# Optimization experiments

Hardware: AMD Instinct MI355X
Metric: run time of the kernel (lower is better)

Reference implementation:

```python
import jax, jax.numpy as jnp
import numpy as np

WINDOW = (16, 16)
STRIDE = (8, 8)
PADDING = (0, 0)  # (pad_h, pad_w), applied symmetrically like torch _pair semantics


def setup_inputs() -> dict:
    key = jax.random.key(0)
    x = jax.random.normal(key, (16, 3, 512, 512), dtype=jnp.float32)
    return {"x": x}


def reference(x) -> jnp.ndarray:
    wh, ww = WINDOW
    sh, sw = STRIDE
    ph, pw = PADDING
    if ph or pw:
        x = jnp.pad(x, ((0, 0), (0, 0), (ph, ph), (pw, pw)))
    B, C, H, W = x.shape
    nH = (H - wh) // sh + 1
    nW = (W - ww) // sw + 1
    # overlapping window gather indices
    rows = (jnp.arange(nH) * sh)[:, None] + jnp.arange(wh)[None, :]  # (nH, wh)
    cols = (jnp.arange(nW) * sw)[:, None] + jnp.arange(ww)[None, :]  # (nW, ww)
    # gather: (B, C, nH, nW, wh, ww)
    p = x[:, :, rows[:, None, :, None], cols[None, :, None, :]]
    # permute to (B, nH, nW, C, wh, ww) then flatten patch grid -> (B, N, C, wh, ww)
    p = jnp.transpose(p, (0, 2, 3, 1, 4, 5))
    return p.reshape(B, nH * nW, C, wh, ww)
```

## Files before the change

kernel.cpp:

```cpp
#include <hip/hip_runtime.h>


#define BB 16
#define CC 3
#define HH 512
#define WW 512
#define NH 63
#define NW 63
#define NP (NH * NW)
#define WIN 16
#define STR 8
#define LDSW 520

typedef float f4 __attribute__((ext_vector_type(4)));

__global__ __launch_bounds__(256) void extract_patches_lds(
    const float* __restrict__ x, float* __restrict__ out) {
  __shared__ float lds[WIN * LDSW];

  unsigned int blk = blockIdx.x;
  unsigned int ph = blk % NH;
  unsigned int t2 = blk / NH;
  unsigned int c  = t2 % CC;
  unsigned int b  = t2 / CC;
  unsigned int tid = threadIdx.x;

  const f4* src = reinterpret_cast<const f4*>(
      x + (((size_t)(b * CC + c) * HH + ph * STR) * WW));
  #pragma unroll
  for (int k = 0; k < 8; ++k) {
    unsigned int idx  = tid + k * 256u;
    f4 v = src[idx];
    unsigned int row  = idx >> 7;
    unsigned int col4 = idx & 127u;
    *reinterpret_cast<f4*>(&lds[row * LDSW + col4 * 4u]) = v;
  }
  __syncthreads();

  f4* dst = reinterpret_cast<f4*>(out) +
            (((size_t)b * NP + (size_t)ph * NW) * CC + c) * 64u;
  for (unsigned int u = tid; u < NW * 64u; u += 256u) {
    unsigned int pw = u >> 6;
    unsigned int r  = u & 63u;
    unsigned int i  = r >> 2;
    unsigned int j4 = r & 3u;
    f4 v = *reinterpret_cast<const f4*>(&lds[i * LDSW + pw * STR + j4 * 4u]);
    __builtin_nontemporal_store(v, &dst[(size_t)pw * (CC * 64u) + r]);
  }
}

extern "C" void kernel_launch(void* const* d_in, const int* in_sizes, int n_in,
                              void* d_out, int out_size, void* d_ws, size_t ws_size,
                              hipStream_t stream) {
  const float* x = (const float*)d_in[0];
  float* out = (float*)d_out;
  dim3 grid(BB * CC * NH);
  extract_patches_lds<<<grid, 256, 0, stream>>>(x, out);
}
```

Baseline: 227.1 us.

## Replace LDS gather with per-element scatter of input to all patch copies

Each thread now loads one float4 of the input exactly once and writes it directly to up to four output positions, the overlapping patches that contain it. The LDS staging, barrier and re-reading of overlapping rows are gone, so total input reads drop to a single pass. In exchange, output writes become scattered 16-byte stores across distant patch addresses instead of contiguous per-row patch runs, which may hurt write coalescing.

```diff
diff --git a/kernel.cpp b/kernel.cpp
--- a/kernel.cpp
+++ b/kernel.cpp
@@ -8,45 +8,43 @@
 #define NH 63
 #define NW 63
 #define NP (NH * NW)
-#define WIN 16
-#define STR 8
-#define LDSW 520
 
 typedef float f4 __attribute__((ext_vector_type(4)));
 
-__global__ __launch_bounds__(256) void extract_patches_lds(
+__global__ __launch_bounds__(256) void scatter_patches(
     const float* __restrict__ x, float* __restrict__ out) {
-  __shared__ float lds[WIN * LDSW];
-
   unsigned int blk = blockIdx.x;
-  unsigned int ph = blk % NH;
-  unsigned int t2 = blk / NH;
-  unsigned int c  = t2 % CC;
-  unsigned int b  = t2 / CC;
   unsigned int tid = threadIdx.x;
 
-  const f4* src = reinterpret_cast<const f4*>(
-      x + (((size_t)(b * CC + c) * HH + ph * STR) * WW));
-  #pragma unroll
-  for (int k = 0; k < 8; ++k) {
-    unsigned int idx  = tid + k * 256u;
-    f4 v = src[idx];
-    unsigned int row  = idx >> 7;
-    unsigned int col4 = idx & 127u;
-    *reinterpret_cast<f4*>(&lds[row * LDSW + col4 * 4u]) = v;
-  }
-  __syncthreads();
+  unsigned int plane = blk >> 8;
+  unsigned int b = plane / CC;
+  unsigned int c = plane - b * CC;
+  unsigned int row  = ((blk & 255u) << 1) | (tid >> 7);
+  unsigned int col4 = tid & 127u;
 
-  f4* dst = reinterpret_cast<f4*>(out) +
-            (((size_t)b * NP + (size_t)ph * NW) * CC + c) * 64u;
-  for (unsigned int u = tid; u < NW * 64u; u += 256u) {
-    unsigned int pw = u >> 6;
-    unsigned int r  = u & 63u;
-    unsigned int i  = r >> 2;
-    unsigned int j4 = r & 3u;
-    f4 v = *reinterpret_cast<const f4*>(&lds[i * LDSW + pw * STR + j4 * 4u]);
-    __builtin_nontemporal_store(v, &dst[(size_t)pw * (CC * 64u) + r]);
-  }
+  const f4* src = reinterpret_cast<const f4*>(x);
+  f4 v = src[(plane << 16) + (row << 7) + col4];
+
+  f4* o = reinterpret_cast<f4*>(out);
+  unsigned int base = b * (NP * CC * 64u) + c * 64u;
+
+  unsigned int ph1 = row >> 3;
+  unsigned int i1  = row & 7u;
+  unsigned int a1 = base + ph1 * (NW * CC * 64u) + (i1 << 2);
+  unsigned int a2 = a1 - (NW * CC * 64u) + 32u;
+
+  unsigned int offA = (col4 >> 1) * (CC * 64u) + (col4 & 1u);
+  unsigned int offB = offA - (CC * 64u) + 2u;
+
+  bool r1 = row < (HH - 8u);
+  bool r2 = row >= 8u;
+  bool ca = col4 < 126u;
+  bool cb = col4 >= 2u;
+
+  if (r1 & ca) __builtin_nontemporal_store(v, &o[a1 + offA]);
+  if (r1 & cb) __builtin_nontemporal_store(v, &o[a1 + offB]);
+  if (r2 & ca) __builtin_nontemporal_store(v, &o[a2 + offA]);
+  if (r2 & cb) __builtin_nontemporal_store(v, &o[a2 + offB]);
 }
 
 extern "C" void kernel_launch(void* const* d_in, const int* in_sizes, int n_in,
@@ -54,6 +52,5 @@
                               hipStream_t stream) {
   const float* x = (const float*)d_in[0];
   float* out = (float*)d_out;
-  dim3 grid(BB * CC * NH);
-  extract_patches_lds<<<grid, 256, 0, stream>>>(x, out);
+  scatter_patches<<<dim3(BB * CC * 256), 256, 0, stream>>>(x, out);
 }
```

Result: slower. 438.6 us (+93.1%).

## Process three patch rows per block with XOR-swizzled LDS and block remapping

Applied to the files above, without the earlier changes.

Each block now loads 32 input rows and emits three overlapping patch rows, so each input row is read once per two patch rows instead of twice. LDS padding is replaced by an XOR swizzle on the column index to avoid bank conflicts, blocks go to 512 threads, and the block index is remapped across 8 groups to spread work. The larger LDS footprint per block may reduce the number of blocks resident per CU.

```diff
diff --git a/kernel.cpp b/kernel.cpp
--- a/kernel.cpp
+++ b/kernel.cpp
@@ -8,44 +8,54 @@
 #define NH 63
 #define NW 63
 #define NP (NH * NW)
-#define WIN 16
-#define STR 8
-#define LDSW 520
+#define G 3
+#define NG (NH / G)
+#define ROWS (8 * G + 8)
+#define TPB 512
 
 typedef float f4 __attribute__((ext_vector_type(4)));
 
-__global__ __launch_bounds__(256) void extract_patches_lds(
+__device__ __forceinline__ unsigned swz(unsigned row, unsigned col4) {
+  return col4 ^ ((row & 3u) << 1);
+}
+
+__global__ __launch_bounds__(TPB) void extract_patches_v3(
     const float* __restrict__ x, float* __restrict__ out) {
-  __shared__ float lds[WIN * LDSW];
+  __shared__ f4 lds[ROWS * 128];
 
-  unsigned int blk = blockIdx.x;
-  unsigned int ph = blk % NH;
-  unsigned int t2 = blk / NH;
-  unsigned int c  = t2 % CC;
-  unsigned int b  = t2 / CC;
-  unsigned int tid = threadIdx.x;
+  unsigned blk = blockIdx.x;
+  unsigned id = (blk & 7u) * (BB * CC * NG / 8u) + (blk >> 3);
 
-  const f4* src = reinterpret_cast<const f4*>(
-      x + (((size_t)(b * CC + c) * HH + ph * STR) * WW));
+  unsigned plane = id / NG;
+  unsigned g = id - plane * NG;
+  unsigned b = plane / CC;
+  unsigned c = plane - b * CC;
+  unsigned tid = threadIdx.x;
+
+  const f4* src = reinterpret_cast<const f4*>(x) +
+                  (((size_t)plane << 9) + 24u * g) * 128u;
   #pragma unroll
   for (int k = 0; k < 8; ++k) {
-    unsigned int idx  = tid + k * 256u;
-    f4 v = src[idx];
-    unsigned int row  = idx >> 7;
-    unsigned int col4 = idx & 127u;
-    *reinterpret_cast<f4*>(&lds[row * LDSW + col4 * 4u]) = v;
+    unsigned idx = tid + (unsigned)k * TPB;
+    unsigned row = idx >> 7;
+    unsigned col4 = idx & 127u;
+    lds[row * 128u + swz(row, col4)] = src[idx];
   }
   __syncthreads();
 
-  f4* dst = reinterpret_cast<f4*>(out) +
-            (((size_t)b * NP + (size_t)ph * NW) * CC + c) * 64u;
-  for (unsigned int u = tid; u < NW * 64u; u += 256u) {
-    unsigned int pw = u >> 6;
-    unsigned int r  = u & 63u;
-    unsigned int i  = r >> 2;
-    unsigned int j4 = r & 3u;
-    f4 v = *reinterpret_cast<const f4*>(&lds[i * LDSW + pw * STR + j4 * 4u]);
-    __builtin_nontemporal_store(v, &dst[(size_t)pw * (CC * 64u) + r]);
+  f4* o = reinterpret_cast<f4*>(out);
+  size_t obase = ((size_t)b * NP + (size_t)(3u * g) * NW) * (CC * 64u) +
+                 (size_t)c * 64u;
+  for (unsigned e = tid; e < 3u * NW * 64u; e += TPB) {
+    unsigned r = e & 63u;
+    unsigned pq = e >> 6;
+    unsigned h = pq / NW;
+    unsigned pw = pq - h * NW;
+    unsigned i = r >> 2;
+    unsigned j4 = r & 3u;
+    unsigned lrow = 8u * h + i;
+    f4 v = lds[lrow * 128u + swz(lrow, 2u * pw + j4)];
+    __builtin_nontemporal_store(v, &o[obase + (size_t)pq * (CC * 64u) + r]);
   }
 }
 
@@ -54,6 +64,5 @@
                               hipStream_t stream) {
   const float* x = (const float*)d_in[0];
   float* out = (float*)d_out;
-  dim3 grid(BB * CC * NH);
-  extract_patches_lds<<<grid, 256, 0, stream>>>(x, out);
+  extract_patches_v3<<<dim3(BB * CC * NG), TPB, 0, stream>>>(x, out);
 }
```

Result: no change. 231.4 us (+1.9%).
